# Kernel optimization log

Measured on AMD Instinct MI355X. Metric: run time of the kernel, lower is better.

Reference implementation:

```python
import jax, jax.numpy as jnp
import numpy as np

N_POINTS = 500000
GRID = 64          # D = H = W
C_VOX = 96         # voxel_feat_dim
C_PT = 32          # point_feat_dim
OFF_DIM = (C_VOX + C_PT) // 2          # 64
DEC_DIM = C_VOX + C_PT + OFF_DIM       # 192


def setup_inputs() -> dict:
    key = jax.random.key(0)
    ks = jax.random.split(key, 10)
    return {
        "voxel_feat": jax.random.normal(ks[0], (C_VOX, GRID, GRID, GRID), jnp.float32),
        "voxel_coords": jax.random.randint(ks[1], (N_POINTS, 3), 0, GRID, jnp.int32),
        "point_feat": jax.random.normal(ks[2], (N_POINTS, C_PT), jnp.float32),
        "point_offsets": jax.random.normal(ks[3], (N_POINTS, 3), jnp.float32),
        # offset_encoder: Linear(3, OFF_DIM), stored as [in, out]
        "W_off": jax.random.normal(ks[4], (3, OFF_DIM), jnp.float32) * 0.1,
        "b_off": jax.random.normal(ks[5], (OFF_DIM,), jnp.float32) * 0.1,
        # decoder MLP: Linear(DEC_DIM, DEC_DIM//2) -> GELU -> Linear(DEC_DIM//2, 3)
        "W1": jax.random.normal(ks[6], (DEC_DIM, DEC_DIM // 2), jnp.float32) * 0.1,
        "b1": jax.random.normal(ks[7], (DEC_DIM // 2,), jnp.float32) * 0.1,
        "W2": jax.random.normal(ks[8], (DEC_DIM // 2, 3), jnp.float32) * 0.1,
        "b2": jax.random.normal(ks[9], (3,), jnp.float32) * 0.1,
    }


def reference(voxel_feat, voxel_coords, point_feat, point_offsets,
              W_off, b_off, W1, b1, W2, b2):
    # Irregular voxel-to-point gather: voxel_feat[:, z, y, x].T -> [N, C_VOX]
    z, y, x = voxel_coords[:, 2], voxel_coords[:, 1], voxel_coords[:, 0]
    voxel_to_point_feat = voxel_feat[:, z, y, x].T  # [N, C_VOX]

    concated = jnp.concatenate([point_feat, voxel_to_point_feat], axis=-1)  # [N, 128]
    offsets_feature = point_offsets @ W_off + b_off                          # [N, 64]
    feat = jnp.concatenate([concated, offsets_feature], axis=-1)            # [N, 192]

    h = jax.nn.gelu(feat @ W1 + b1, approximate=False)  # torch nn.GELU is exact erf
    flow = h @ W2 + b2                                   # [N, 3]
    return flow
```

## Files before the change

kernel.cpp:

```cpp
#include <hip/hip_runtime.h>
#include <math.h>

#define NPTS   500000
#define GRIDW  64
#define NVOX   (GRIDW*GRIDW*GRIDW)
#define C_VOXC 96
#define C_PTC  32
#define OFFD   64
#define HID    96
#define HHALF  48

__device__ __forceinline__ float gelu_fast(float s) {
    const float u  = s * 0.70710678118654752440f;
    const float au = fabsf(u);
    const float t  = __fdividef(1.0f, fmaf(0.3275911f, au, 1.0f));
    float p = fmaf(1.061405429f, t, -1.453152027f);
    p = fmaf(p, t, 1.421413741f);
    p = fmaf(p, t, -0.284496736f);
    p = fmaf(p, t, 0.254829592f);
    p *= t;
    const float e = __expf(-u * u);
    float r = fmaf(-p, e, 1.0f);
    r = copysignf(r, u);
    return 0.5f * s * (1.0f + r);
}

__global__ void fold_kernel(const float* __restrict__ W_off,
                            const float* __restrict__ b_off,
                            const float* __restrict__ W1,
                            const float* __restrict__ b1,
                            float* __restrict__ Wc,
                            float* __restrict__ bcomb) {
    int j = threadIdx.x;
    if (j >= HID) return;
    float bc = b1[j];
    float w0 = 0.f, w1 = 0.f, w2 = 0.f;
    for (int d = 0; d < OFFD; ++d) {
        float w = W1[(C_PTC + C_VOXC + d) * HID + j];
        bc += b_off[d] * w;
        w0 = fmaf(W_off[0 * OFFD + d], w, w0);
        w1 = fmaf(W_off[1 * OFFD + d], w, w1);
        w2 = fmaf(W_off[2 * OFFD + d], w, w2);
    }
    Wc[0 * HID + j] = w0;
    Wc[1 * HID + j] = w1;
    Wc[2 * HID + j] = w2;
    bcomb[j] = bc;
}

__global__ __launch_bounds__(256) void voxgemm_kernel(
        const float* __restrict__ vf,
        const float* __restrict__ W1,
        float* __restrict__ vc) {
    const int v = blockIdx.x * 256 + threadIdx.x;
    const float* __restrict__ W1v = W1 + C_PTC * HID;

    float acc[HID];
#pragma unroll
    for (int j = 0; j < HID; ++j) acc[j] = 0.f;

    for (int c = 0; c < C_VOXC; ++c) {
        float a = vf[(size_t)c * NVOX + v];
#pragma unroll
        for (int j = 0; j < HID; ++j)
            acc[j] = fmaf(a, W1v[c * HID + j], acc[j]);
    }

    float* __restrict__ dst = vc + (size_t)v * HID;
#pragma unroll
    for (int j = 0; j < HID; j += 4) {
        float4 st = make_float4(acc[j], acc[j + 1], acc[j + 2], acc[j + 3]);
        *reinterpret_cast<float4*>(&dst[j]) = st;
    }
}

__global__ __launch_bounds__(256) void point_kernel(
        const int* __restrict__ coords,
        const float* __restrict__ pf,
        const float* __restrict__ po,
        const float* __restrict__ W1,
        const float* __restrict__ W2,
        const float* __restrict__ b2,
        const float* __restrict__ Wc,
        const float* __restrict__ bcomb,
        const float* __restrict__ vc,
        float* __restrict__ out) {
    const int i = blockIdx.x * 256 + threadIdx.x;
    if (i >= NPTS) return;

    const int x = coords[i * 3 + 0];
    const int y = coords[i * 3 + 1];
    const int z = coords[i * 3 + 2];
    const int vidx = (z * GRIDW + y) * GRIDW + x;
    const float4* __restrict__ vrow4 =
        reinterpret_cast<const float4*>(vc + (size_t)vidx * HID);

    float4 vrA[12];
#pragma unroll
    for (int q = 0; q < 12; ++q) vrA[q] = vrow4[q];

    const float o0 = po[i * 3 + 0];
    const float o1 = po[i * 3 + 1];
    const float o2 = po[i * 3 + 2];

    float pfr[C_PTC];
    {
        const float4* __restrict__ p4 =
            reinterpret_cast<const float4*>(pf + (size_t)i * C_PTC);
#pragma unroll
        for (int q = 0; q < 8; ++q) {
            float4 v = p4[q];
            pfr[4 * q + 0] = v.x; pfr[4 * q + 1] = v.y;
            pfr[4 * q + 2] = v.z; pfr[4 * q + 3] = v.w;
        }
    }

    float f0 = b2[0], f1 = b2[1], f2 = b2[2];
    float4 vrB[12];

#pragma unroll
    for (int h = 0; h < 2; ++h) {
        const int j0 = h * HHALF;
        float acc[HHALF];

#pragma unroll
        for (int j = 0; j < HHALF; ++j) {
            float a = fmaf(o2, Wc[2 * HID + j0 + j], bcomb[j0 + j]);
            a = fmaf(o1, Wc[1 * HID + j0 + j], a);
            acc[j] = fmaf(o0, Wc[0 * HID + j0 + j], a);
        }

#pragma unroll
        for (int k = 0; k < C_PTC; ++k) {
            const float fk = pfr[k];
            const float* __restrict__ wrow = W1 + k * HID + j0;
#pragma unroll
            for (int j = 0; j < HHALF; ++j)
                acc[j] = fmaf(fk, wrow[j], acc[j]);
        }

        if (h == 0) {
#pragma unroll
            for (int q = 0; q < 12; ++q) {
                acc[4 * q + 0] += vrA[q].x;
                acc[4 * q + 1] += vrA[q].y;
                acc[4 * q + 2] += vrA[q].z;
                acc[4 * q + 3] += vrA[q].w;
            }
#pragma unroll
            for (int q = 0; q < 12; ++q) vrB[q] = vrow4[12 + q];
        } else {
#pragma unroll
            for (int q = 0; q < 12; ++q) {
                acc[4 * q + 0] += vrB[q].x;
                acc[4 * q + 1] += vrB[q].y;
                acc[4 * q + 2] += vrB[q].z;
                acc[4 * q + 3] += vrB[q].w;
            }
        }

#pragma unroll
        for (int j = 0; j < HHALF; ++j) {
            const float hh = gelu_fast(acc[j]);
            f0 = fmaf(hh, W2[(j0 + j) * 3 + 0], f0);
            f1 = fmaf(hh, W2[(j0 + j) * 3 + 1], f1);
            f2 = fmaf(hh, W2[(j0 + j) * 3 + 2], f2);
        }
    }

    out[i * 3 + 0] = f0;
    out[i * 3 + 1] = f1;
    out[i * 3 + 2] = f2;
}

__global__ __launch_bounds__(256) void point_direct_kernel(
        const int* __restrict__ coords,
        const float* __restrict__ vf,
        const float* __restrict__ pf,
        const float* __restrict__ po,
        const float* __restrict__ W1,
        const float* __restrict__ W2,
        const float* __restrict__ b2,
        const float* __restrict__ Wc,
        const float* __restrict__ bcomb,
        float* __restrict__ out) {
    const int i = blockIdx.x * 256 + threadIdx.x;
    if (i >= NPTS) return;

    const int x = coords[i * 3 + 0];
    const int y = coords[i * 3 + 1];
    const int z = coords[i * 3 + 2];
    const int vidx = (z * GRIDW + y) * GRIDW + x;

    float acc[HID];
#pragma unroll
    for (int j = 0; j < HID; ++j) acc[j] = bcomb[j];

    const float* __restrict__ W1v = W1 + C_PTC * HID;
    for (int c = 0; c < C_VOXC; ++c) {
        const float a = vf[(size_t)c * NVOX + vidx];
#pragma unroll
        for (int j = 0; j < HID; ++j)
            acc[j] = fmaf(a, W1v[c * HID + j], acc[j]);
    }

    const float o0 = po[i * 3 + 0];
    const float o1 = po[i * 3 + 1];
    const float o2 = po[i * 3 + 2];
#pragma unroll
    for (int j = 0; j < HID; ++j) {
        float a = fmaf(o2, Wc[2 * HID + j], acc[j]);
        a = fmaf(o1, Wc[1 * HID + j], a);
        acc[j] = fmaf(o0, Wc[0 * HID + j], a);
    }

    const float* __restrict__ pfr = pf + (size_t)i * C_PTC;
    for (int k = 0; k < C_PTC; ++k) {
        const float fk = pfr[k];
#pragma unroll
        for (int j = 0; j < HID; ++j)
            acc[j] = fmaf(fk, W1[k * HID + j], acc[j]);
    }

    float f0 = b2[0], f1 = b2[1], f2 = b2[2];
#pragma unroll
    for (int j = 0; j < HID; ++j) {
        const float hh = gelu_fast(acc[j]);
        f0 = fmaf(hh, W2[j * 3 + 0], f0);
        f1 = fmaf(hh, W2[j * 3 + 1], f1);
        f2 = fmaf(hh, W2[j * 3 + 2], f2);
    }

    out[i * 3 + 0] = f0;
    out[i * 3 + 1] = f1;
    out[i * 3 + 2] = f2;
}

extern "C" void kernel_launch(void* const* d_in, const int* in_sizes, int n_in,
                              void* d_out, int out_size, void* d_ws, size_t ws_size,
                              hipStream_t stream) {
    const float* vf    = (const float*)d_in[0];
    const int*   vcrd  = (const int*)  d_in[1];
    const float* pf    = (const float*)d_in[2];
    const float* po    = (const float*)d_in[3];
    const float* W_off = (const float*)d_in[4];
    const float* b_off = (const float*)d_in[5];
    const float* W1    = (const float*)d_in[6];
    const float* b1    = (const float*)d_in[7];
    const float* W2    = (const float*)d_in[8];
    const float* b2    = (const float*)d_in[9];
    float* out = (float*)d_out;

    float* Wc    = (float*)d_ws;
    float* bcomb = Wc + 384;
    float* vcb   = Wc + 1024;

    const size_t need = (size_t)(1024 + (size_t)NVOX * HID) * sizeof(float);

    fold_kernel<<<1, 128, 0, stream>>>(W_off, b_off, W1, b1, Wc, bcomb);

    if (ws_size >= need) {
        voxgemm_kernel<<<NVOX / 256, 256, 0, stream>>>(vf, W1, vcb);
        point_kernel<<<(NPTS + 255) / 256, 256, 0, stream>>>(
            vcrd, pf, po, W1, W2, b2, Wc, bcomb, vcb, out);
    } else {
        point_direct_kernel<<<(NPTS + 255) / 256, 256, 0, stream>>>(
            vcrd, vf, pf, po, W1, W2, b2, Wc, bcomb, out);
    }
}
```

Measured before the change: 376.6 us.

## Store precomputed voxel projections as bf16 and batch channel loads

```diff
diff --git a/kernel.cpp b/kernel.cpp
--- a/kernel.cpp
+++ b/kernel.cpp
@@ -9,6 +9,18 @@
 #define OFFD   64
 #define HID    96
 #define HHALF  48
+
+__device__ __forceinline__ unsigned f2bf(float f) {
+    unsigned u = __float_as_uint(f);
+    unsigned r = u + 0x7fffu + ((u >> 16) & 1u);
+    return r >> 16;
+}
+__device__ __forceinline__ float bflo(unsigned u) {
+    return __uint_as_float(u << 16);
+}
+__device__ __forceinline__ float bfhi(unsigned u) {
+    return __uint_as_float(u & 0xffff0000u);
+}
 
 __device__ __forceinline__ float gelu_fast(float s) {
     const float u  = s * 0.70710678118654752440f;
@@ -48,10 +60,10 @@
     bcomb[j] = bc;
 }
 
-__global__ __launch_bounds__(256) void voxgemm_kernel(
+__global__ __launch_bounds__(256, 2) void voxgemm_kernel(
         const float* __restrict__ vf,
         const float* __restrict__ W1,
-        float* __restrict__ vc) {
+        uint4* __restrict__ vc) {
     const int v = blockIdx.x * 256 + threadIdx.x;
     const float* __restrict__ W1v = W1 + C_PTC * HID;
 
@@ -59,18 +71,30 @@
 #pragma unroll
     for (int j = 0; j < HID; ++j) acc[j] = 0.f;
 
-    for (int c = 0; c < C_VOXC; ++c) {
-        float a = vf[(size_t)c * NVOX + v];
-#pragma unroll
-        for (int j = 0; j < HID; ++j)
-            acc[j] = fmaf(a, W1v[c * HID + j], acc[j]);
-    }
-
-    float* __restrict__ dst = vc + (size_t)v * HID;
-#pragma unroll
-    for (int j = 0; j < HID; j += 4) {
-        float4 st = make_float4(acc[j], acc[j + 1], acc[j + 2], acc[j + 3]);
-        *reinterpret_cast<float4*>(&dst[j]) = st;
+#pragma unroll 1
+    for (int c = 0; c < C_VOXC; c += 8) {
+        float a[8];
+#pragma unroll
+        for (int t = 0; t < 8; ++t)
+            a[t] = vf[(size_t)(c + t) * NVOX + v];
+#pragma unroll
+        for (int t = 0; t < 8; ++t) {
+            const float* __restrict__ wrow = W1v + (c + t) * HID;
+#pragma unroll
+            for (int j = 0; j < HID; ++j)
+                acc[j] = fmaf(a[t], wrow[j], acc[j]);
+        }
+    }
+
+    uint4* __restrict__ d4 = vc + (size_t)v * 12;
+#pragma unroll
+    for (int k = 0; k < 12; ++k) {
+        const int j = k * 8;
+        unsigned a0 = f2bf(acc[j + 0]) | (f2bf(acc[j + 1]) << 16);
+        unsigned a1 = f2bf(acc[j + 2]) | (f2bf(acc[j + 3]) << 16);
+        unsigned a2 = f2bf(acc[j + 4]) | (f2bf(acc[j + 5]) << 16);
+        unsigned a3 = f2bf(acc[j + 6]) | (f2bf(acc[j + 7]) << 16);
+        d4[k] = make_uint4(a0, a1, a2, a3);
     }
 }
 
@@ -83,7 +107,7 @@
         const float* __restrict__ b2,
         const float* __restrict__ Wc,
         const float* __restrict__ bcomb,
-        const float* __restrict__ vc,
+        const uint4* __restrict__ vc,
         float* __restrict__ out) {
     const int i = blockIdx.x * 256 + threadIdx.x;
     if (i >= NPTS) return;
@@ -92,12 +116,11 @@
     const int y = coords[i * 3 + 1];
     const int z = coords[i * 3 + 2];
     const int vidx = (z * GRIDW + y) * GRIDW + x;
-    const float4* __restrict__ vrow4 =
-        reinterpret_cast<const float4*>(vc + (size_t)vidx * HID);
-
-    float4 vrA[12];
-#pragma unroll
-    for (int q = 0; q < 12; ++q) vrA[q] = vrow4[q];
+    const uint4* __restrict__ vrow = vc + (size_t)vidx * 12;
+
+    uint4 vrA[6];
+#pragma unroll
+    for (int q = 0; q < 6; ++q) vrA[q] = vrow[q];
 
     const float o0 = po[i * 3 + 0];
     const float o1 = po[i * 3 + 1];
@@ -116,7 +139,7 @@
     }
 
     float f0 = b2[0], f1 = b2[1], f2 = b2[2];
-    float4 vrB[12];
+    uint4 vrB[6];
 
 #pragma unroll
     for (int h = 0; h < 2; ++h) {
@@ -139,24 +162,22 @@
                 acc[j] = fmaf(fk, wrow[j], acc[j]);
         }
 
+        const uint4* g = (h == 0) ? vrA : vrB;
         if (h == 0) {
 #pragma unroll
-            for (int q = 0; q < 12; ++q) {
-                acc[4 * q + 0] += vrA[q].x;
-                acc[4 * q + 1] += vrA[q].y;
-                acc[4 * q + 2] += vrA[q].z;
-                acc[4 * q + 3] += vrA[q].w;
-            }
-#pragma unroll
-            for (int q = 0; q < 12; ++q) vrB[q] = vrow4[12 + q];
-        } else {
-#pragma unroll
-            for (int q = 0; q < 12; ++q) {
-                acc[4 * q + 0] += vrB[q].x;
-                acc[4 * q + 1] += vrB[q].y;
-                acc[4 * q + 2] += vrB[q].z;
-                acc[4 * q + 3] += vrB[q].w;
-            }
+            for (int q = 0; q < 6; ++q) vrB[q] = vrow[6 + q];
+        }
+#pragma unroll
+        for (int q = 0; q < 6; ++q) {
+            const unsigned a0 = g[q].x, a1 = g[q].y, a2 = g[q].z, a3 = g[q].w;
+            acc[8 * q + 0] += bflo(a0);
+            acc[8 * q + 1] += bfhi(a0);
+            acc[8 * q + 2] += bflo(a1);
+            acc[8 * q + 3] += bfhi(a1);
+            acc[8 * q + 4] += bflo(a2);
+            acc[8 * q + 5] += bfhi(a2);
+            acc[8 * q + 6] += bflo(a3);
+            acc[8 * q + 7] += bfhi(a3);
         }
 
 #pragma unroll
@@ -253,9 +274,9 @@
 
     float* Wc    = (float*)d_ws;
     float* bcomb = Wc + 384;
-    float* vcb   = Wc + 1024;
-
-    const size_t need = (size_t)(1024 + (size_t)NVOX * HID) * sizeof(float);
+    uint4* vcb   = reinterpret_cast<uint4*>((char*)d_ws + 4096);
+
+    const size_t need = 4096 + (size_t)NVOX * HID * sizeof(unsigned short);
 
     fold_kernel<<<1, 128, 0, stream>>>(W_off, b_off, W1, b1, Wc, bcomb);
 
```

Result: slower. 611.5 us (+62.4%).
